# Kernel optimization log

Hardware: AMD Instinct MI355X
Metric: run time of the kernel (lower is better)

Reference implementation:

```python
import jax, jax.numpy as jnp
import numpy as np

N_CODES = 8192
CODE_DIM = 256
COMMITMENT_COST = 0.25
EMA_DECAY = 0.99
EPS = 1e-5


def setup_inputs() -> dict:
    key = jax.random.key(0)
    k1, k2 = jax.random.split(key)
    B, N, D, K = 8, 2048, CODE_DIM, N_CODES
    z = jax.random.normal(k1, (B, N, D), dtype=jnp.float32)
    # torch init: uniform(-1/n_codes, 1/n_codes); use small-scale init for realism
    emb_weight = jax.random.uniform(k2, (K, D), minval=-1.0 / K, maxval=1.0 / K, dtype=jnp.float32)
    return {
        "z": z,
        "emb_weight": emb_weight,
        "ema_cluster_size": jnp.zeros((K,), jnp.float32),
        "ema_w": jnp.zeros((K, D), jnp.float32),
        "code_usage": jnp.zeros((K,), jnp.float32),
    }


def reference(z, emb_weight, ema_cluster_size, ema_w, code_usage):
    # training=True path of VectorQuantizerV2.forward
    B, N, D = z.shape
    K = emb_weight.shape[0]
    z_flat = z.reshape(-1, D)  # [T, D], T = B*N

    # squared L2 distances: ||z||^2 + ||e||^2 - 2 z e^T  -> [T, K]
    d = (jnp.sum(z_flat * z_flat, axis=1, keepdims=True)
         + jnp.sum(emb_weight * emb_weight, axis=1)
         - 2.0 * z_flat @ emb_weight.T)
    idx = jnp.argmin(d, axis=-1)  # [T] int32

    z_q = emb_weight[idx].reshape(B, N, D)

    # usage tracking (scatter-add of ones == segment counts)
    cluster_size = jax.ops.segment_sum(jnp.ones_like(idx, jnp.float32), idx, num_segments=K)
    new_code_usage = code_usage + cluster_size

    # EMA codebook update (no one-hot materialization; segment_sum == encodings.T @ z)
    new_ecs = ema_cluster_size * EMA_DECAY + (1.0 - EMA_DECAY) * cluster_size
    n = jnp.sum(new_ecs)
    new_ecs = (new_ecs + EPS) / (n + K * EPS) * n  # Laplace smoothing
    dw = jax.ops.segment_sum(z_flat, idx, num_segments=K)  # [K, D]
    new_ema_w = ema_w * EMA_DECAY + (1.0 - EMA_DECAY) * dw
    new_emb_weight = new_ema_w / jnp.clip(new_ecs, EPS, None)[:, None]

    # losses (computed with z_q from the OLD codebook, matching torch op order)
    commitment_loss = jnp.mean((z - jax.lax.stop_gradient(z_q)) ** 2)
    codebook_loss = jnp.mean((z_q - jax.lax.stop_gradient(z)) ** 2)
    vq_loss = COMMITMENT_COST * commitment_loss + codebook_loss

    # straight-through estimator
    z_q_out = z + jax.lax.stop_gradient(z_q - z)

    # perplexity from empirical code distribution of this batch
    avg_probs = cluster_size / (B * N)
    perplexity = jnp.exp(-jnp.sum(avg_probs * jnp.log(avg_probs + 1e-10)))

    unique_codes = jnp.sum(new_code_usage > 0).astype(jnp.float32)
    usage_ratio = unique_codes / K

    indices = idx.reshape(B, N)
    return (z_q_out, indices, vq_loss, perplexity, usage_ratio, unique_codes,
            new_emb_weight, new_ecs, new_ema_w, new_code_usage)
```

## Files before the change

kernel.cpp:

```cpp
#include <hip/hip_runtime.h>
#include <hip/hip_bf16.h>
#include <math.h>

#define TOKS 16384
#define DDIM 256
#define KC   8192

static constexpr float EMA   = 0.99f;
static constexpr float ONE_M = (float)(1.0 - 0.99);
static constexpr float EPSF  = 1e-5f;
static constexpr float KEPS  = (float)(8192 * 1e-5);

#define CTILE  32
#define CAP    128
#define DELTA  2.0e-4f

#define CS_OFF    0
#define SCAL_OFF  8192
#define AN_OFF    8208
#define BN_OFF    24592
#define CNT_OFF   41?
#undef CNT_OFF
#define CNT_OFF   32784
#define GMX_OFF   49168
#define EB_OFF    65552
#define LISTS_OFF 1114128

typedef __attribute__((ext_vector_type(8))) short bf16x8;
typedef __attribute__((ext_vector_type(4))) short bf16x4;
typedef __attribute__((ext_vector_type(4))) float f32x4;

static __device__ inline short f2b(float f) {
  __hip_bfloat16 h = __float2bfloat16(f);
  return *reinterpret_cast<short*>(&h);
}
static __device__ inline unsigned int fkey(float f) {
  unsigned int b = __float_as_uint(f);
  return (b & 0x80000000u) ? ~b : (b | 0x80000000u);
}
static __device__ inline float funkey(unsigned int k) {
  unsigned int b = (k & 0x80000000u) ? (k & 0x7FFFFFFFu) : ~k;
  return __uint_as_float(b);
}

__global__ __launch_bounds__(256) void k_conv(const float* __restrict__ e,
                                              const float* __restrict__ z,
                                              unsigned short* __restrict__ eb,
                                              unsigned short* __restrict__ zb,
                                              float* __restrict__ bn,
                                              float* __restrict__ an) {
  const int lane = threadIdx.x & 63;
  const int row = blockIdx.x * 4 + (threadIdx.x >> 6);
  const bool isE = row < KC;
  const float* src = isE ? e : z;
  unsigned short* dst = isE ? eb : zb;
  float* nrm = isE ? bn : an;
  const int r = isE ? row : row - KC;
  const float4 v = *reinterpret_cast<const float4*>(src + (size_t)r * DDIM + lane * 4);
  bf16x4 b;
  b[0] = f2b(v.x); b[1] = f2b(v.y); b[2] = f2b(v.z); b[3] = f2b(v.w);
  *reinterpret_cast<bf16x4*>(dst + (size_t)r * DDIM + lane * 4) = b;
  float s = v.x * v.x + v.y * v.y + v.z * v.z + v.w * v.w;
#pragma unroll
  for (int d = 32; d; d >>= 1) s += __shfl_down(s, d);
  if (lane == 0) nrm[r] = s;
}

template<bool COLLECT>
__global__ __launch_bounds__(256, 4) void k_screen(
    const unsigned short* __restrict__ zb, const unsigned short* __restrict__ eb,
    unsigned int* __restrict__ gmx,
    unsigned int* __restrict__ cnt, unsigned short* __restrict__ lists) {
  constexpr int CHUNKC = COLLECT ? 1024 : 256;
  constexpr int NITC = CHUNKC / CTILE;
  __shared__ unsigned short Bt[2][CTILE * 256];

  const int tid = threadIdx.x;
  const int lane = tid & 63;
  const int w = tid >> 6;
  const int t0 = blockIdx.x * 128;
  const int k0 = blockIdx.y * CHUNKC;

  bf16x8 a[2][8];
  {
    const int rlo = lane & 15;
    const int khi = (lane >> 4) * 8;
#pragma unroll
    for (int rf = 0; rf < 2; ++rf) {
      const unsigned short* zr =
          zb + (size_t)(t0 + w * 32 + rf * 16 + rlo) * DDIM + khi;
#pragma unroll
      for (int kk = 0; kk < 8; ++kk)
        a[rf][kk] = *reinterpret_cast<const bf16x8*>(zr + kk * 32);
    }
  }

  float tr[2][4];
  float rm[2][4];
#pragma unroll
  for (int rf = 0; rf < 2; ++rf)
#pragma unroll
    for (int r = 0; r < 4; ++r) {
      rm[rf][r] = -1e30f;
      if (COLLECT)
        tr[rf][r] = funkey(gmx[t0 + w * 32 + rf * 16 + (lane >> 4) * 4 + r]) - DELTA;
    }

  const char* ebB = reinterpret_cast<const char*>(eb);
  const int sc = tid >> 3;
  const int ss = tid & 7;
  const int swz = (sc & 7) << 4;

  {
    const size_t gb = (size_t)(k0 + sc) * 512 + ss * 16;
    char* dst = reinterpret_cast<char*>(&Bt[0][0]) + sc * 512;
#pragma unroll
    for (int q = 0; q < 4; ++q) {
      const uint4 g = *reinterpret_cast<const uint4*>(ebB + gb + q * 128);
      *reinterpret_cast<uint4*>(dst + ((ss * 16 + q * 128) ^ swz)) = g;
    }
  }
  __syncthreads();

  const int rdlo = lane & 15;
  const int rdhi = (lane >> 4) * 16;
  uint4 g[4];

  for (int ct = 0; ct < NITC; ++ct) {
    if (ct + 1 < NITC) {
      const size_t gb = (size_t)(k0 + (ct + 1) * CTILE + sc) * 512 + ss * 16;
#pragma unroll
      for (int q = 0; q < 4; ++q)
        g[q] = *reinterpret_cast<const uint4*>(ebB + gb + q * 128);
    }

    f32x4 acc[2][2];
#pragma unroll
    for (int rf = 0; rf < 2; ++rf)
#pragma unroll
      for (int cf = 0; cf < 2; ++cf) acc[rf][cf] = (f32x4){0.f, 0.f, 0.f, 0.f};

    const char* buf = reinterpret_cast<const char*>(&Bt[ct & 1][0]);
#pragma unroll
    for (int kk = 0; kk < 8; ++kk) {
      const int off = (kk * 64 + rdhi) ^ ((rdlo & 7) << 4);
      const bf16x8 b0 = *reinterpret_cast<const bf16x8*>(buf + rdlo * 512 + off);
      const bf16x8 b1 = *reinterpret_cast<const bf16x8*>(buf + (16 + rdlo) * 512 + off);
      acc[0][0] = __builtin_amdgcn_mfma_f32_16x16x32_bf16(a[0][kk], b0, acc[0][0], 0, 0, 0);
      acc[1][0] = __builtin_amdgcn_mfma_f32_16x16x32_bf16(a[1][kk], b0, acc[1][0], 0, 0, 0);
      acc[0][1] = __builtin_amdgcn_mfma_f32_16x16x32_bf16(a[0][kk], b1, acc[0][1], 0, 0, 0);
      acc[1][1] = __builtin_amdgcn_mfma_f32_16x16x32_bf16(a[1][kk], b1, acc[1][1], 0, 0, 0);
    }

    if (!COLLECT) {
#pragma unroll
      for (int rf = 0; rf < 2; ++rf)
#pragma unroll
        for (int r = 0; r < 4; ++r)
          rm[rf][r] = fmaxf(rm[rf][r], fmaxf(acc[rf][0][r], acc[rf][1][r]));
    } else {
      const int kb = k0 + ct * CTILE;
#pragma unroll
      for (int rf = 0; rf < 2; ++rf) {
#pragma unroll
        for (int r = 0; r < 4; ++r) {
          const float th = tr[rf][r];
          if (acc[rf][0][r] >= th || acc[rf][1][r] >= th) {
            const int t = t0 + w * 32 + rf * 16 + (lane >> 4) * 4 + r;
            if (acc[rf][0][r] >= th) {
              const unsigned int o_ = atomicAdd(&cnt[t], 1u);
              if (o_ < CAP) lists[(size_t)t * CAP + o_] = (unsigned short)(kb + rdlo);
            }
            if (acc[rf][1][r] >= th) {
              const unsigned int o_ = atomicAdd(&cnt[t], 1u);
              if (o_ < CAP) lists[(size_t)t * CAP + o_] = (unsigned short)(kb + 16 + rdlo);
            }
          }
        }
      }
    }

    if (ct + 1 < NITC) {
      char* dst = reinterpret_cast<char*>(&Bt[(ct + 1) & 1][0]) + sc * 512;
#pragma unroll
      for (int q = 0; q < 4; ++q)
        *reinterpret_cast<uint4*>(dst + ((ss * 16 + q * 128) ^ swz)) = g[q];
    }
    __syncthreads();
  }

  if (!COLLECT) {
#pragma unroll
    for (int rf = 0; rf < 2; ++rf) {
#pragma unroll
      for (int r = 0; r < 4; ++r) {
        float v = rm[rf][r];
#pragma unroll
        for (int o = 1; o <= 8; o <<= 1) v = fmaxf(v, __shfl_xor(v, o));
        if ((lane & 15) == 0) {
          const int t = t0 + w * 32 + rf * 16 + (lane >> 4) * 4 + r;
          atomicMax(&gmx[t], fkey(v));
        }
      }
    }
  }
}

__global__ __launch_bounds__(256) void k_rescore(
    const float* __restrict__ z, const float* __restrict__ emb,
    const float* __restrict__ an, const float* __restrict__ bn,
    const unsigned int* __restrict__ cnt, const unsigned short* __restrict__ lists,
    float* __restrict__ out_idx, float* __restrict__ o0,
    float* __restrict__ o8, float* __restrict__ cs, float* __restrict__ scal) {
  const int w = threadIdx.x >> 6;
  const int lane = threadIdx.x & 63;
  const int t = blockIdx.x * 4 + w;

  const float4 z4 = *reinterpret_cast<const float4*>(z + (size_t)t * DDIM + lane * 4);
  const unsigned int nraw = cnt[t];
  const float aN = an[t];
  float bd = 3.4e38f;
  int bk = 0x7fffffff;

  if (nraw <= CAP) {
    const int n = (int)nraw;
    for (int c = 0; c < n; ++c) {
      const int k = (int)lists[(size_t)t * CAP + c];
      const float4 e4 = *reinterpret_cast<const float4*>(emb + (size_t)k * DDIM + lane * 4);
      float p = z4.x * e4.x + z4.y * e4.y + z4.z * e4.z + z4.w * e4.w;
#pragma unroll
      for (int o = 32; o; o >>= 1) p += __shfl_xor(p, o);
      const float d = __fsub_rn(__fadd_rn(aN, bn[k]), __fmul_rn(2.0f, p));
      if (d < bd || (d == bd && k < bk)) { bd = d; bk = k; }
    }
  } else {
    for (int kb = 0; kb < KC; kb += 4) {
      float p0, p1, p2, p3;
      {
        const float4 e0 = *reinterpret_cast<const float4*>(emb + (size_t)(kb + 0) * DDIM + lane * 4);
        const float4 e1 = *reinterpret_cast<const float4*>(emb + (size_t)(kb + 1) * DDIM + lane * 4);
        const float4 e2 = *reinterpret_cast<const float4*>(emb + (size_t)(kb + 2) * DDIM + lane * 4);
        const float4 e3 = *reinterpret_cast<const float4*>(emb + (size_t)(kb + 3) * DDIM + lane * 4);
        p0 = z4.x * e0.x + z4.y * e0.y + z4.z * e0.z + z4.w * e0.w;
        p1 = z4.x * e1.x + z4.y * e1.y + z4.z * e1.z + z4.w * e1.w;
        p2 = z4.x * e2.x + z4.y * e2.y + z4.z * e2.z + z4.w * e2.w;
        p3 = z4.x * e3.x + z4.y * e3.y + z4.z * e3.z + z4.w * e3.w;
      }
#pragma unroll
      for (int o = 32; o; o >>= 1) {
        p0 += __shfl_xor(p0, o);
        p1 += __shfl_xor(p1, o);
        p2 += __shfl_xor(p2, o);
        p3 += __shfl_xor(p3, o);
      }
      const float d0 = __fsub_rn(__fadd_rn(aN, bn[kb + 0]), __fmul_rn(2.0f, p0));
      const float d1 = __fsub_rn(__fadd_rn(aN, bn[kb + 1]), __fmul_rn(2.0f, p1));
      const float d2 = __fsub_rn(__fadd_rn(aN, bn[kb + 2]), __fmul_rn(2.0f, p2));
      const float d3 = __fsub_rn(__fadd_rn(aN, bn[kb + 3]), __fmul_rn(2.0f, p3));
      if (d0 < bd) { bd = d0; bk = kb + 0; }
      if (d1 < bd) { bd = d1; bk = kb + 1; }
      if (d2 < bd) { bd = d2; bk = kb + 2; }
      if (d3 < bd) { bd = d3; bk = kb + 3; }
    }
  }

  if (lane == 0) out_idx[t] = (float)bk;

  const float4 ev = *reinterpret_cast<const float4*>(emb + (size_t)bk * DDIM + lane * 4);
  float4 o;
  o.x = __fadd_rn(z4.x, __fsub_rn(ev.x, z4.x));
  o.y = __fadd_rn(z4.y, __fsub_rn(ev.y, z4.y));
  o.z = __fadd_rn(z4.z, __fsub_rn(ev.z, z4.z));
  o.w = __fadd_rn(z4.w, __fsub_rn(ev.w, z4.w));
  *reinterpret_cast<float4*>(o0 + (size_t)t * DDIM + lane * 4) = o;
  const float dx = __fsub_rn(z4.x, ev.x);
  const float dy = __fsub_rn(z4.y, ev.y);
  const float dz = __fsub_rn(z4.z, ev.z);
  const float dw = __fsub_rn(z4.w, ev.w);
  float lsum = dx * dx + dy * dy + dz * dz + dw * dw;
  float* dst = o8 + (size_t)bk * DDIM + lane * 4;
  unsafeAtomicAdd(dst + 0, ONE_M * z4.x);
  unsafeAtomicAdd(dst + 1, ONE_M * z4.y);
  unsafeAtomicAdd(dst + 2, ONE_M * z4.z);
  unsafeAtomicAdd(dst + 3, ONE_M * z4.w);
  if (lane == 0) atomicAdd(cs + bk, 1.0f);

#pragma unroll
  for (int o_ = 32; o_; o_ >>= 1) lsum += __shfl_down(lsum, o_);
  __shared__ float wsum[4];
  if (lane == 0) wsum[w] = lsum;
  __syncthreads();
  if (threadIdx.x == 0)
    atomicAdd(scal + 0, wsum[0] + wsum[1] + wsum[2] + wsum[3]);
}

__global__ __launch_bounds__(256) void k_scale_ema(const float* __restrict__ ema_w,
                                                   float* __restrict__ o8) {
  const size_t i = ((size_t)blockIdx.x * 256 + threadIdx.x) * 4;
  const float4 v = *reinterpret_cast<const float4*>(ema_w + i);
  float4 r;
  r.x = EMA * v.x; r.y = EMA * v.y; r.z = EMA * v.z; r.w = EMA * v.w;
  *reinterpret_cast<float4*>(o8 + i) = r;
}

__global__ __launch_bounds__(256) void k_stats(const float* __restrict__ ecs_in,
                                               const float* __restrict__ cu_in,
                                               const float* __restrict__ cs,
                                               float* __restrict__ o7,
                                               float* __restrict__ o9,
                                               float* __restrict__ scal) {
  const int k = blockIdx.x * 256 + threadIdx.x;
  const int w = threadIdx.x >> 6;
  const int lane = threadIdx.x & 63;
  const float cc = cs[k];
  const float raw = EMA * ecs_in[k] + ONE_M * cc;
  o7[k] = raw;
  const float ncu = __fadd_rn(cu_in[k], cc);
  o9[k] = ncu;
  const float p = cc * (1.0f / 16384.0f);
  float s0 = raw;
  float s1 = p * logf(p + 1e-10f);
  float s2 = ncu > 0.0f ? 1.0f : 0.0f;
#pragma unroll
  for (int o = 32; o; o >>= 1) {
    s0 += __shfl_down(s0, o);
    s1 += __shfl_down(s1, o);
    s2 += __shfl_down(s2, o);
  }
  __shared__ float w0[4], w1[4], w2[4];
  if (lane == 0) { w0[w] = s0; w1[w] = s1; w2[w] = s2; }
  __syncthreads();
  if (threadIdx.x == 0) {
    atomicAdd(scal + 1, w0[0] + w0[1] + w0[2] + w0[3]);
    atomicAdd(scal + 2, w1[0] + w1[1] + w1[2] + w1[3]);
    atomicAdd(scal + 3, w2[0] + w2[1] + w2[2] + w2[3]);
  }
}

__global__ __launch_bounds__(256) void k_final(float* __restrict__ o7,
                                               const float* __restrict__ o8,
                                               const float* __restrict__ scal,
                                               float* __restrict__ o6,
                                               float* __restrict__ o2,
                                               float* __restrict__ o3,
                                               float* __restrict__ o4,
                                               float* __restrict__ o5) {
  const int lane = threadIdx.x & 63;
  const int k = blockIdx.x * 4 + (threadIdx.x >> 6);
  const float n = scal[1];
  const float raw = o7[k];
  const float sm = (raw + EPSF) / (n + KEPS) * n;
  if (lane == 0) o7[k] = sm;
  const float dnm = fmaxf(sm, EPSF);
  const size_t i = (size_t)k * DDIM + lane * 4;
  const float4 v = *reinterpret_cast<const float4*>(o8 + i);
  float4 r;
  r.x = v.x / dnm; r.y = v.y / dnm; r.z = v.z / dnm; r.w = v.w / dnm;
  *reinterpret_cast<float4*>(o6 + i) = r;
  if (blockIdx.x == 0 && threadIdx.x == 0) {
    const float m = scal[0] * (1.0f / 4194304.0f);
    o2[0] = 0.25f * m + m;
    o3[0] = expf(-scal[2]);
    o4[0] = scal[3] * (1.0f / 8192.0f);
    o5[0] = scal[3];
  }
}

extern "C" void kernel_launch(void* const* d_in, const int* in_sizes, int n_in,
                              void* d_out, int out_size, void* d_ws, size_t ws_size,
                              hipStream_t stream) {
  const float* z     = (const float*)d_in[0];
  const float* emb   = (const float*)d_in[1];
  const float* ecs   = (const float*)d_in[2];
  const float* ema_w = (const float*)d_in[3];
  const float* cu    = (const float*)d_in[4];

  float* out = (float*)d_out;
  float* o0 = out;
  float* o1 = o0 + 4194304;
  float* o2 = o1 + 16384;
  float* o3 = o2 + 1;
  float* o4 = o3 + 1;
  float* o5 = o4 + 1;
  float* o6 = o5 + 1;
  float* o7 = o6 + 2097152;
  float* o8 = o7 + 8192;
  float* o9 = o8 + 2097152;

  float* w    = (float*)d_ws;
  float* cs   = w + CS_OFF;
  float* scal = w + SCAL_OFF;
  float* an   = w + AN_OFF;
  float* bn   = w + BN_OFF;
  unsigned int* cnt = (unsigned int*)(w + CNT_OFF);
  unsigned int* gmx = (unsigned int*)(w + GMX_OFF);
  unsigned short* eb = (unsigned short*)(w + EB_OFF);
  unsigned short* lists = (unsigned short*)(w + LISTS_OFF);
  unsigned short* zb = (unsigned short*)o0;

  hipMemsetAsync(w + CS_OFF, 0, (8192 + 16) * sizeof(float), stream);
  hipMemsetAsync(w + CNT_OFF, 0, 2 * TOKS * sizeof(unsigned int), stream);

  k_conv<<<(KC + TOKS) / 4, 256, 0, stream>>>(emb, z, eb, zb, bn, an);

  k_screen<false><<<dim3(TOKS / 128, 8), 256, 0, stream>>>(zb, eb, gmx, cnt, lists);
  k_screen<true><<<dim3(TOKS / 128, 8), 256, 0, stream>>>(zb, eb, gmx, cnt, lists);

  k_scale_ema<<<(KC * DDIM) / 1024, 256, 0, stream>>>(ema_w, o8);
  k_rescore<<<TOKS / 4, 256, 0, stream>>>(z, emb, an, bn, cnt, lists, o1, o0, o8, cs, scal);

  k_stats<<<KC / 256, 256, 0, stream>>>(ecs, cu, cs, o7, o9, scal);
  k_final<<<KC / 4, 256, 0, stream>>>(o7, o8, scal, o6, o2, o3, o4, o5);
}
```

Baseline: 266.2 us.

## Replace float atomic segment-sum with counting-sort scatter and per-code gather

The EMA dw segment-sum used to be float atomics into o8 from every token, after a separate pass that pre-scaled ema_w. Now rescore records each index and an integer count, and a scan, scatter and gather sequence builds per-code token lists. Each code's row is then summed directly and fused with the EMA update and the stats. This removes 4M float atomics and the separate scale and stats kernels, at the cost of three extra small launches and a single-block scan.

```diff
diff --git a/kernel.cpp b/kernel.cpp
--- a/kernel.cpp
+++ b/kernel.cpp
@@ -15,16 +15,18 @@
 #define CAP    128
 #define DELTA  2.0e-4f
 
-#define CS_OFF    0
-#define SCAL_OFF  8192
-#define AN_OFF    8208
-#define BN_OFF    24592
-#define CNT_OFF   41?
-#undef CNT_OFF
-#define CNT_OFF   32784
-#define GMX_OFF   49168
-#define EB_OFF    65552
-#define LISTS_OFF 1114128
+#define SCAL_OFF  0
+#define UCNT_OFF  16
+#define FILL_OFF  8208
+#define CNT_OFF   16400
+#define GMX_OFF   32784
+#define AN_OFF    49168
+#define BN_OFF    65552
+#define IDXI_OFF  73744
+#define BASE_OFF  90128
+#define TOK_OFF   98320
+#define EB_OFF    106512
+#define LISTS_OFF 1155088
 
 typedef __attribute__((ext_vector_type(8))) short bf16x8;
 typedef __attribute__((ext_vector_type(4))) short bf16x4;
@@ -210,8 +212,9 @@
     const float* __restrict__ z, const float* __restrict__ emb,
     const float* __restrict__ an, const float* __restrict__ bn,
     const unsigned int* __restrict__ cnt, const unsigned short* __restrict__ lists,
-    float* __restrict__ out_idx, float* __restrict__ o0,
-    float* __restrict__ o8, float* __restrict__ cs, float* __restrict__ scal) {
+    float* __restrict__ out_idx, int* __restrict__ idxi,
+    float* __restrict__ o0, unsigned int* __restrict__ ucnt,
+    float* __restrict__ scal) {
   const int w = threadIdx.x >> 6;
   const int lane = threadIdx.x & 63;
   const int t = blockIdx.x * 4 + w;
@@ -264,7 +267,11 @@
     }
   }
 
-  if (lane == 0) out_idx[t] = (float)bk;
+  if (lane == 0) {
+    out_idx[t] = (float)bk;
+    idxi[t] = bk;
+    atomicAdd(&ucnt[bk], 1u);
+  }
 
   const float4 ev = *reinterpret_cast<const float4*>(emb + (size_t)bk * DDIM + lane * 4);
   float4 o;
@@ -278,13 +285,6 @@
   const float dz = __fsub_rn(z4.z, ev.z);
   const float dw = __fsub_rn(z4.w, ev.w);
   float lsum = dx * dx + dy * dy + dz * dz + dw * dw;
-  float* dst = o8 + (size_t)bk * DDIM + lane * 4;
-  unsafeAtomicAdd(dst + 0, ONE_M * z4.x);
-  unsafeAtomicAdd(dst + 1, ONE_M * z4.y);
-  unsafeAtomicAdd(dst + 2, ONE_M * z4.z);
-  unsafeAtomicAdd(dst + 3, ONE_M * z4.w);
-  if (lane == 0) atomicAdd(cs + bk, 1.0f);
-
 #pragma unroll
   for (int o_ = 32; o_; o_ >>= 1) lsum += __shfl_down(lsum, o_);
   __shared__ float wsum[4];
@@ -294,46 +294,82 @@
     atomicAdd(scal + 0, wsum[0] + wsum[1] + wsum[2] + wsum[3]);
 }
 
-__global__ __launch_bounds__(256) void k_scale_ema(const float* __restrict__ ema_w,
-                                                   float* __restrict__ o8) {
-  const size_t i = ((size_t)blockIdx.x * 256 + threadIdx.x) * 4;
-  const float4 v = *reinterpret_cast<const float4*>(ema_w + i);
-  float4 r;
-  r.x = EMA * v.x; r.y = EMA * v.y; r.z = EMA * v.z; r.w = EMA * v.w;
-  *reinterpret_cast<float4*>(o8 + i) = r;
-}
-
-__global__ __launch_bounds__(256) void k_stats(const float* __restrict__ ecs_in,
-                                               const float* __restrict__ cu_in,
-                                               const float* __restrict__ cs,
-                                               float* __restrict__ o7,
-                                               float* __restrict__ o9,
-                                               float* __restrict__ scal) {
-  const int k = blockIdx.x * 256 + threadIdx.x;
+__global__ __launch_bounds__(256) void k_scan(const unsigned int* __restrict__ ucnt,
+                                              unsigned int* __restrict__ base) {
+  __shared__ unsigned int part[256];
+  const int tid = threadIdx.x;
+  unsigned int loc[32];
+  unsigned int s = 0;
+#pragma unroll
+  for (int i = 0; i < 32; ++i) { loc[i] = s; s += ucnt[tid * 32 + i]; }
+  part[tid] = s;
+  __syncthreads();
+  if (tid == 0) {
+    unsigned int run = 0;
+    for (int j = 0; j < 256; ++j) { const unsigned int v = part[j]; part[j] = run; run += v; }
+  }
+  __syncthreads();
+  const unsigned int b = part[tid];
+#pragma unroll
+  for (int i = 0; i < 32; ++i) base[tid * 32 + i] = b + loc[i];
+}
+
+__global__ __launch_bounds__(256) void k_scatter(const int* __restrict__ idxi,
+                                                 const unsigned int* __restrict__ base,
+                                                 unsigned int* __restrict__ fill,
+                                                 unsigned short* __restrict__ tok) {
+  const int t = blockIdx.x * 256 + threadIdx.x;
+  const int k = idxi[t];
+  const unsigned int p = atomicAdd(&fill[k], 1u);
+  tok[base[k] + p] = (unsigned short)t;
+}
+
+__global__ __launch_bounds__(256) void k_gather(
+    const float* __restrict__ z, const float* __restrict__ ema_w,
+    const unsigned int* __restrict__ ucnt, const unsigned int* __restrict__ base,
+    const unsigned short* __restrict__ tok,
+    const float* __restrict__ ecs_in, const float* __restrict__ cu_in,
+    float* __restrict__ o8, float* __restrict__ o7, float* __restrict__ o9,
+    float* __restrict__ scal) {
   const int w = threadIdx.x >> 6;
   const int lane = threadIdx.x & 63;
-  const float cc = cs[k];
-  const float raw = EMA * ecs_in[k] + ONE_M * cc;
-  o7[k] = raw;
-  const float ncu = __fadd_rn(cu_in[k], cc);
-  o9[k] = ncu;
-  const float p = cc * (1.0f / 16384.0f);
-  float s0 = raw;
-  float s1 = p * logf(p + 1e-10f);
-  float s2 = ncu > 0.0f ? 1.0f : 0.0f;
-#pragma unroll
-  for (int o = 32; o; o >>= 1) {
-    s0 += __shfl_down(s0, o);
-    s1 += __shfl_down(s1, o);
-    s2 += __shfl_down(s2, o);
-  }
-  __shared__ float w0[4], w1[4], w2[4];
-  if (lane == 0) { w0[w] = s0; w1[w] = s1; w2[w] = s2; }
+  const int k = blockIdx.x * 4 + w;
+  const unsigned int c = ucnt[k];
+  const unsigned int b = base[k];
+
+  float4 sum = {0.f, 0.f, 0.f, 0.f};
+  for (unsigned int i = 0; i < c; ++i) {
+    const int t = (int)tok[b + i];
+    const float4 zv = *reinterpret_cast<const float4*>(z + (size_t)t * DDIM + lane * 4);
+    sum.x += zv.x; sum.y += zv.y; sum.z += zv.z; sum.w += zv.w;
+  }
+  const float4 ew = *reinterpret_cast<const float4*>(ema_w + (size_t)k * DDIM + lane * 4);
+  float4 r;
+  r.x = EMA * ew.x + ONE_M * sum.x;
+  r.y = EMA * ew.y + ONE_M * sum.y;
+  r.z = EMA * ew.z + ONE_M * sum.z;
+  r.w = EMA * ew.w + ONE_M * sum.w;
+  *reinterpret_cast<float4*>(o8 + (size_t)k * DDIM + lane * 4) = r;
+
+  float s0 = 0.f, s1 = 0.f, s2 = 0.f;
+  if (lane == 0) {
+    const float cc = (float)c;
+    const float raw = EMA * ecs_in[k] + ONE_M * cc;
+    o7[k] = raw;
+    const float ncu = __fadd_rn(cu_in[k], cc);
+    o9[k] = ncu;
+    s0 = raw;
+    const float p = cc * (1.0f / 16384.0f);
+    s1 = p * logf(p + 1e-10f);
+    s2 = ncu > 0.0f ? 1.0f : 0.0f;
+  }
+  __shared__ float sh0[4], sh1[4], sh2[4];
+  if (lane == 0) { sh0[w] = s0; sh1[w] = s1; sh2[w] = s2; }
   __syncthreads();
   if (threadIdx.x == 0) {
-    atomicAdd(scal + 1, w0[0] + w0[1] + w0[2] + w0[3]);
-    atomicAdd(scal + 2, w1[0] + w1[1] + w1[2] + w1[3]);
-    atomicAdd(scal + 3, w2[0] + w2[1] + w2[2] + w2[3]);
+    atomicAdd(scal + 1, sh0[0] + sh0[1] + sh0[2] + sh0[3]);
+    atomicAdd(scal + 2, sh1[0] + sh1[1] + sh1[2] + sh1[3]);
+    atomicAdd(scal + 3, sh2[0] + sh2[1] + sh2[2] + sh2[3]);
   }
 }
 
@@ -388,27 +424,34 @@
   float* o9 = o8 + 2097152;
 
   float* w    = (float*)d_ws;
-  float* cs   = w + CS_OFF;
   float* scal = w + SCAL_OFF;
+  unsigned int* ucnt = (unsigned int*)(w + UCNT_OFF);
+  unsigned int* fill = (unsigned int*)(w + FILL_OFF);
+  unsigned int* cnt  = (unsigned int*)(w + CNT_OFF);
+  unsigned int* gmx  = (unsigned int*)(w + GMX_OFF);
   float* an   = w + AN_OFF;
   float* bn   = w + BN_OFF;
-  unsigned int* cnt = (unsigned int*)(w + CNT_OFF);
-  unsigned int* gmx = (unsigned int*)(w + GMX_OFF);
-  unsigned short* eb = (unsigned short*)(w + EB_OFF);
+  int*   idxi = (int*)(w + IDXI_OFF);
+  unsigned int* base = (unsigned int*)(w + BASE_OFF);
+  unsigned short* tok = (unsigned short*)(w + TOK_OFF);
+  unsigned short* eb  = (unsigned short*)(w + EB_OFF);
   unsigned short* lists = (unsigned short*)(w + LISTS_OFF);
   unsigned short* zb = (unsigned short*)o0;
 
-  hipMemsetAsync(w + CS_OFF, 0, (8192 + 16) * sizeof(float), stream);
-  hipMemsetAsync(w + CNT_OFF, 0, 2 * TOKS * sizeof(unsigned int), stream);
+  hipMemsetAsync(w, 0, (size_t)(GMX_OFF + TOKS) * sizeof(float) - 0, stream);
 
   k_conv<<<(KC + TOKS) / 4, 256, 0, stream>>>(emb, z, eb, zb, bn, an);
 
   k_screen<false><<<dim3(TOKS / 128, 8), 256, 0, stream>>>(zb, eb, gmx, cnt, lists);
   k_screen<true><<<dim3(TOKS / 128, 8), 256, 0, stream>>>(zb, eb, gmx, cnt, lists);
 
-  k_scale_ema<<<(KC * DDIM) / 1024, 256, 0, stream>>>(ema_w, o8);
-  k_rescore<<<TOKS / 4, 256, 0, stream>>>(z, emb, an, bn, cnt, lists, o1, o0, o8, cs, scal);
-
-  k_stats<<<KC / 256, 256, 0, stream>>>(ecs, cu, cs, o7, o9, scal);
+  k_rescore<<<TOKS / 4, 256, 0, stream>>>(z, emb, an, bn, cnt, lists,
+                                          o1, idxi, o0, ucnt, scal);
+
+  k_scan<<<1, 256, 0, stream>>>(ucnt, base);
+  k_scatter<<<TOKS / 256, 256, 0, stream>>>(idxi, base, fill, tok);
+  k_gather<<<KC / 4, 256, 0, stream>>>(z, ema_w, ucnt, base, tok, ecs, cu,
+                                       o8, o7, o9, scal);
+
   k_final<<<KC / 4, 256, 0, stream>>>(o7, o8, scal, o6, o2, o3, o4, o5);
 }
```

Result: slower. 319.8 us (+20.1%).
